# Kernel tuning notes

Measured on AMD Instinct MI355X. Metric: run time of the kernel, lower is better.

## Reference

```python
import jax, jax.numpy as jnp
import numpy as np

NFEATURES = 8192
NPCAS = 256
SIGMA = 16.0
COEFF_NORM = np.sqrt(NPCAS) / SIGMA  # = 1.0
FEAT_NORM = np.sqrt(2.0 / NFEATURES)
TWO_PI = 2.0 * np.pi


def fwht(x):
    """Normalized fast Walsh-Hadamard transform along the last axis (power of 2)."""
    d = x.shape[-1]
    h = 1
    while h < d:
        y = x.reshape(*x.shape[:-1], d // (2 * h), 2, h)
        a, b = y[..., 0, :], y[..., 1, :]
        x = jnp.stack([a + b, a - b], axis=-2).reshape(*x.shape)
        h *= 2
    return x * (d ** -0.5)


def setup_inputs() -> dict:
    key = jax.random.key(0)
    k = jax.random.split(key, 6)
    M, A, R = 32, 64, 512
    S = 4
    nstacks = NFEATURES // NPCAS
    rep = jax.random.normal(k[0], (M, A, R), dtype=jnp.float32)
    charges = jax.random.randint(k[1], (M, A), 0, S, dtype=jnp.int32)
    reductors = jax.random.normal(k[2], (S, R, NPCAS), dtype=jnp.float32)
    Dmat = jax.random.normal(k[3], (S, 1, nstacks, NPCAS), dtype=jnp.float32)
    bias = jax.random.uniform(k[4], (S, NFEATURES), dtype=jnp.float32) * TWO_PI
    alpha = jax.random.normal(k[5], (NFEATURES,), dtype=jnp.float32)
    return {"rep": rep, "charges": charges, "reductors": reductors,
            "Dmat": Dmat, "bias": bias, "alpha": alpha}


def reference(rep, charges, reductors, Dmat, bias, alpha):
    M, A, R = rep.shape
    S, _, P = reductors.shape
    ntransforms, nstacks = Dmat.shape[1], Dmat.shape[2]
    F = nstacks * P
    D = jnp.where(Dmat >= 0, 1.0, -1.0).astype(rep.dtype)  # +-1 SORF diagonals
    Z = jnp.zeros((M, F), dtype=rep.dtype)
    for s in range(S):
        # PCA projection: [M, A, P]
        proj = jnp.einsum('mar,rp->map', rep, reductors[s])
        # replicate across stacks: [M, A, nstacks, P]
        x = jnp.broadcast_to(proj[:, :, None, :], (M, A, nstacks, P))
        for t in range(ntransforms):
            x = fwht(D[s, t] * x)
        coeffs = COEFF_NORM * x.reshape(M, A, F)
        feats = jnp.cos(coeffs + bias[s])
        mask = (charges == s)[..., None]  # species membership per atom
        Z = Z + FEAT_NORM * jnp.sum(jnp.where(mask, feats, 0.0), axis=1)
    return Z @ alpha  # [M] out-of-sample predictions
```

## Files before the change

kernel.cpp:

```cpp
#include <hip/hip_runtime.h>

#define NATOMS 2048
#define R_DIM 512
#define P_DIM 256
#define S_DIM 4
#define NSTACKS 32
#define F_DIM 8192
#define KS 8
#define KSPAN (R_DIM / KS)
#define TR 64
#define TC 128
#define KT 16
#define RT_TILES 11

#define DPPF(x, ctrl) \
  __int_as_float(__builtin_amdgcn_update_dpp( \
      __float_as_int(x), __float_as_int(x), (ctrl), 0xF, 0xF, false))


__global__ __launch_bounds__(256) void sorf_proj_kernel(
    const float* __restrict__ rep, const float* __restrict__ reductors,
    const int* __restrict__ charges, float* __restrict__ projp,
    float* __restrict__ out) {
  int bid = blockIdx.x;
  int ks = bid & 7;
  int cb = (bid >> 3) & 1;
  int r2 = bid >> 4;
  int rt = r2 % RT_TILES;
  int s  = r2 / RT_TILES;

  int t = threadIdx.x;
  int lane = t & 63, wave = t >> 6;
  if (bid == 0 && t < 32) out[t] = 0.f;

  __shared__ int rowsL[TR];
  __shared__ int wtot[4];
  int4 c0v = ((const int4*)charges)[t * 2];
  int4 c1v = ((const int4*)charges)[t * 2 + 1];
  int fl[8];
  fl[0] = (c0v.x == s); fl[1] = (c0v.y == s); fl[2] = (c0v.z == s); fl[3] = (c0v.w == s);
  fl[4] = (c1v.x == s); fl[5] = (c1v.y == s); fl[6] = (c1v.z == s); fl[7] = (c1v.w == s);
  int cnt8 = ((fl[0] + fl[1]) + (fl[2] + fl[3])) + ((fl[4] + fl[5]) + (fl[6] + fl[7]));
  int scan = cnt8;
#pragma unroll
  for (int o = 1; o < 64; o <<= 1) {
    int y = __shfl_up(scan, o);
    if (lane >= o) scan += y;
  }
  if (lane == 63) wtot[wave] = scan;
  __syncthreads();
  int wb = 0;
#pragma unroll
  for (int w = 0; w < 4; ++w) wb += (w < wave) ? wtot[w] : 0;
  int total = (wtot[0] + wtot[1]) + (wtot[2] + wtot[3]);
  int lo = rt * TR;
  int nrows = min(TR, total - lo);
  if (nrows <= 0) return;
  if (t >= nrows && t < TR) rowsL[t] = 0;
  int pos = wb + scan - cnt8;
#pragma unroll
  for (int i = 0; i < 8; ++i) {
    if (fl[i]) {
      int rel = pos - lo;
      if (rel >= 0 && rel < TR) rowsL[rel] = t * 8 + i;
      pos++;
    }
  }
  __syncthreads();

  __shared__ float As[KT][TR + 4];
  __shared__ float Bs[KT][TC];

  int ar = t >> 2;
  int aq = t & 3;
  const float* aSrc = rep + (size_t)rowsL[ar] * R_DIM + ks * KSPAN + aq * 4;
  int kb = t >> 4;
  int cc = (t & 15) * 4;
  const float* bSrc = reductors + ((size_t)s * R_DIM + ks * KSPAN + kb) * P_DIM + cb * TC + cc;

  int ty = t >> 4, tx = t & 15;
  int r0 = ty * 4;
  int c0 = tx * 4;

  float acc[4][8];
#pragma unroll
  for (int i = 0; i < 4; ++i)
#pragma unroll
    for (int j = 0; j < 8; ++j) acc[i][j] = 0.f;

  float4 a  = *(const float4*)aSrc;
  float4 b0 = *(const float4*)bSrc;
  float4 b1 = *(const float4*)(bSrc + 64);

#pragma unroll 1
  for (int k0 = 0; k0 < KSPAN; k0 += KT) {
    __syncthreads();
    As[aq * 4 + 0][ar] = a.x;
    As[aq * 4 + 1][ar] = a.y;
    As[aq * 4 + 2][ar] = a.z;
    As[aq * 4 + 3][ar] = a.w;
    *(float4*)&Bs[kb][cc] = b0;
    *(float4*)&Bs[kb][cc + 64] = b1;
    __syncthreads();
    if (k0 + KT < KSPAN) {
      a  = *(const float4*)(aSrc + k0 + KT);
      b0 = *(const float4*)(bSrc + (size_t)(k0 + KT) * P_DIM);
      b1 = *(const float4*)(bSrc + (size_t)(k0 + KT) * P_DIM + 64);
    }
#pragma unroll
    for (int kk = 0; kk < KT; ++kk) {
      float4 aV = *(const float4*)&As[kk][r0];
      float4 bA = *(const float4*)&Bs[kk][c0];
      float4 bB = *(const float4*)&Bs[kk][c0 + 64];
      float av[4] = {aV.x, aV.y, aV.z, aV.w};
      float bv[8] = {bA.x, bA.y, bA.z, bA.w, bB.x, bB.y, bB.z, bB.w};
#pragma unroll
      for (int i = 0; i < 4; ++i)
#pragma unroll
        for (int j = 0; j < 8; ++j) acc[i][j] = fmaf(av[i], bv[j], acc[i][j]);
    }
  }

#pragma unroll
  for (int i = 0; i < 4; ++i) {
    int r = r0 + i;
    if (r < nrows) {
      float* dst = projp + ((size_t)ks * NATOMS + rowsL[r]) * P_DIM + cb * TC + c0;
      *(float4*)dst = make_float4(acc[i][0], acc[i][1], acc[i][2], acc[i][3]);
      *(float4*)(dst + 64) = make_float4(acc[i][4], acc[i][5], acc[i][6], acc[i][7]);
    }
  }
}

__global__ __launch_bounds__(256) void sorf_feat_kernel(
    const float* __restrict__ projp, const int* __restrict__ charges,
    const float* __restrict__ Dmat, const float* __restrict__ bias,
    const float* __restrict__ alpha, float* __restrict__ out) {
  const int atom = blockIdx.x;
  const int t = threadIdx.x;
  const int lane = t & 63;
  const int wave = t >> 6;
  const int s = charges[atom];

  float4 p = *((const float4*)(projp + (size_t)atom * P_DIM) + lane);
#pragma unroll
  for (int ksi = 1; ksi < KS; ++ksi) {
    float4 q = *((const float4*)(projp + ((size_t)ksi * NATOMS + atom) * P_DIM) + lane);
    p.x += q.x; p.y += q.y; p.z += q.z; p.w += q.w;
  }

  const float sg1  = (lane & 1)  ? -1.f : 1.f;
  const float sg2  = (lane & 2)  ? -1.f : 1.f;
  const float sg4  = (lane & 4)  ? -1.f : 1.f;
  const float sg8  = (lane & 8)  ? -1.f : 1.f;
  const float sg16 = (lane & 16) ? -1.f : 1.f;
  const float sg32 = (lane & 32) ? -1.f : 1.f;
  const bool hi4 = (lane & 4) != 0;

  const float* Db = Dmat + (size_t)s * (NSTACKS * P_DIM);
  const float* bb = bias + (size_t)s * F_DIM;
  float accum = 0.f;

#pragma unroll 2
  for (int j = wave * 8; j < wave * 8 + 8; ++j) {
    float4 d  = *((const float4*)(Db + j * P_DIM) + lane);
    float4 bi = *((const float4*)(bb + j * P_DIM) + lane);
    float4 al = *((const float4*)(alpha + j * P_DIM) + lane);
    float x0 = (d.x >= 0.f) ? p.x : -p.x;
    float x1 = (d.y >= 0.f) ? p.y : -p.y;
    float x2 = (d.z >= 0.f) ? p.z : -p.z;
    float x3 = (d.w >= 0.f) ? p.w : -p.w;
    float t0 = x0 + x1, t1 = x0 - x1, t2 = x2 + x3, t3 = x2 - x3;
    x0 = t0 + t2; x2 = t0 - t2; x1 = t1 + t3; x3 = t1 - t3;
    { float y0 = DPPF(x0, 0xB1), y1 = DPPF(x1, 0xB1), y2 = DPPF(x2, 0xB1), y3 = DPPF(x3, 0xB1);
      x0 = fmaf(sg1, x0, y0); x1 = fmaf(sg1, x1, y1);
      x2 = fmaf(sg1, x2, y2); x3 = fmaf(sg1, x3, y3); }
    { float y0 = DPPF(x0, 0x4E), y1 = DPPF(x1, 0x4E), y2 = DPPF(x2, 0x4E), y3 = DPPF(x3, 0x4E);
      x0 = fmaf(sg2, x0, y0); x1 = fmaf(sg2, x1, y1);
      x2 = fmaf(sg2, x2, y2); x3 = fmaf(sg2, x3, y3); }
    { float a0 = DPPF(x0, 0x104), a1 = DPPF(x1, 0x104), a2 = DPPF(x2, 0x104), a3 = DPPF(x3, 0x104);
      float b0 = DPPF(x0, 0x114), b1 = DPPF(x1, 0x114), b2 = DPPF(x2, 0x114), b3 = DPPF(x3, 0x114);
      float y0 = hi4 ? b0 : a0;
      float y1 = hi4 ? b1 : a1;
      float y2 = hi4 ? b2 : a2;
      float y3 = hi4 ? b3 : a3;
      x0 = fmaf(sg4, x0, y0); x1 = fmaf(sg4, x1, y1);
      x2 = fmaf(sg4, x2, y2); x3 = fmaf(sg4, x3, y3); }
    { float y0 = DPPF(x0, 0x128), y1 = DPPF(x1, 0x128), y2 = DPPF(x2, 0x128), y3 = DPPF(x3, 0x128);
      x0 = fmaf(sg8, x0, y0); x1 = fmaf(sg8, x1, y1);
      x2 = fmaf(sg8, x2, y2); x3 = fmaf(sg8, x3, y3); }
    { float y0 = __shfl_xor(x0, 16), y1 = __shfl_xor(x1, 16),
            y2 = __shfl_xor(x2, 16), y3 = __shfl_xor(x3, 16);
      x0 = fmaf(sg16, x0, y0); x1 = fmaf(sg16, x1, y1);
      x2 = fmaf(sg16, x2, y2); x3 = fmaf(sg16, x3, y3); }
    { float y0 = __shfl_xor(x0, 32), y1 = __shfl_xor(x1, 32),
            y2 = __shfl_xor(x2, 32), y3 = __shfl_xor(x3, 32);
      x0 = fmaf(sg32, x0, y0); x1 = fmaf(sg32, x1, y1);
      x2 = fmaf(sg32, x2, y2); x3 = fmaf(sg32, x3, y3); }
    accum += __cosf(fmaf(x0, 0.0625f, bi.x)) * al.x;
    accum += __cosf(fmaf(x1, 0.0625f, bi.y)) * al.y;
    accum += __cosf(fmaf(x2, 0.0625f, bi.z)) * al.z;
    accum += __cosf(fmaf(x3, 0.0625f, bi.w)) * al.w;
  }

  accum += DPPF(accum, 0xB1);
  accum += DPPF(accum, 0x4E);
  accum += DPPF(accum, 0x124);
  accum += DPPF(accum, 0x128);
  accum += __shfl_xor(accum, 16);
  accum += __shfl_xor(accum, 32);

  __shared__ float wsum[4];
  if (lane == 0) wsum[wave] = accum;
  __syncthreads();
  if (t == 0) {
    atomicAdd(out + (atom >> 6), 0.015625f * ((wsum[0] + wsum[1]) + (wsum[2] + wsum[3])));
  }
}

extern "C" void kernel_launch(void* const* d_in, const int* in_sizes, int n_in,
                              void* d_out, int out_size, void* d_ws, size_t ws_size,
                              hipStream_t stream) {
  const float* rep       = (const float*)d_in[0];
  const int*   charges   = (const int*)d_in[1];
  const float* reductors = (const float*)d_in[2];
  const float* Dmat      = (const float*)d_in[3];
  const float* bias      = (const float*)d_in[4];
  const float* alpha     = (const float*)d_in[5];
  float* out = (float*)d_out;

  float* projp = (float*)((char*)d_ws + 16384);

  sorf_proj_kernel<<<8 * 2 * RT_TILES * S_DIM, 256, 0, stream>>>(
      rep, reductors, charges, projp, out);
  sorf_feat_kernel<<<NATOMS, 256, 0, stream>>>(projp, charges, Dmat, bias, alpha, out);
}
```

Before: 111.0 us.

## Fuse projection and feature kernels into one persistent kernel with grid barrier

Merges the projection GEMM kernel and the SORF feature kernel into a single launch of 704 blocks. A global atomic counter barrier separates the phases, and a memset resets the counter on every call. After the barrier each wave handles one whole atom across all 32 stacks, instead of one block per atom split over four waves. This removes a kernel launch gap and the tail drain between the two kernels. In exchange it adds a memset, a spin barrier that depends on all 704 blocks being co-resident (launch bounds set to 3 blocks per CU), and longer per-wave serial work in the second phase.

Measured after the change: 318.4 us. 2.87x slower.

```diff
diff --git a/kernel.cpp b/kernel.cpp
--- a/kernel.cpp
+++ b/kernel.cpp
@@ -12,209 +12,222 @@
 #define TC 128
 #define KT 16
 #define RT_TILES 11
+#define NTILES (8 * 2 * RT_TILES * S_DIM)
 
 #define DPPF(x, ctrl) \
   __int_as_float(__builtin_amdgcn_update_dpp( \
       __float_as_int(x), __float_as_int(x), (ctrl), 0xF, 0xF, false))
 
 
-__global__ __launch_bounds__(256) void sorf_proj_kernel(
+__global__ __launch_bounds__(256, 3) void sorf_one_kernel(
     const float* __restrict__ rep, const float* __restrict__ reductors,
-    const int* __restrict__ charges, float* __restrict__ projp,
+    const int* __restrict__ charges, const float* __restrict__ Dmat,
+    const float* __restrict__ bias, const float* __restrict__ alpha,
+    float* __restrict__ projp, unsigned* __restrict__ bar,
     float* __restrict__ out) {
-  int bid = blockIdx.x;
-  int ks = bid & 7;
-  int cb = (bid >> 3) & 1;
-  int r2 = bid >> 4;
-  int rt = r2 % RT_TILES;
-  int s  = r2 / RT_TILES;
-
-  int t = threadIdx.x;
-  int lane = t & 63, wave = t >> 6;
-  if (bid == 0 && t < 32) out[t] = 0.f;
-
   __shared__ int rowsL[TR];
   __shared__ int wtot[4];
-  int4 c0v = ((const int4*)charges)[t * 2];
-  int4 c1v = ((const int4*)charges)[t * 2 + 1];
-  int fl[8];
-  fl[0] = (c0v.x == s); fl[1] = (c0v.y == s); fl[2] = (c0v.z == s); fl[3] = (c0v.w == s);
-  fl[4] = (c1v.x == s); fl[5] = (c1v.y == s); fl[6] = (c1v.z == s); fl[7] = (c1v.w == s);
-  int cnt8 = ((fl[0] + fl[1]) + (fl[2] + fl[3])) + ((fl[4] + fl[5]) + (fl[6] + fl[7]));
-  int scan = cnt8;
-#pragma unroll
-  for (int o = 1; o < 64; o <<= 1) {
-    int y = __shfl_up(scan, o);
-    if (lane >= o) scan += y;
-  }
-  if (lane == 63) wtot[wave] = scan;
-  __syncthreads();
-  int wb = 0;
-#pragma unroll
-  for (int w = 0; w < 4; ++w) wb += (w < wave) ? wtot[w] : 0;
-  int total = (wtot[0] + wtot[1]) + (wtot[2] + wtot[3]);
-  int lo = rt * TR;
-  int nrows = min(TR, total - lo);
-  if (nrows <= 0) return;
-  if (t >= nrows && t < TR) rowsL[t] = 0;
-  int pos = wb + scan - cnt8;
-#pragma unroll
-  for (int i = 0; i < 8; ++i) {
-    if (fl[i]) {
-      int rel = pos - lo;
-      if (rel >= 0 && rel < TR) rowsL[rel] = t * 8 + i;
-      pos++;
-    }
-  }
-  __syncthreads();
-
   __shared__ float As[KT][TR + 4];
   __shared__ float Bs[KT][TC];
 
-  int ar = t >> 2;
-  int aq = t & 3;
-  const float* aSrc = rep + (size_t)rowsL[ar] * R_DIM + ks * KSPAN + aq * 4;
-  int kb = t >> 4;
-  int cc = (t & 15) * 4;
-  const float* bSrc = reductors + ((size_t)s * R_DIM + ks * KSPAN + kb) * P_DIM + cb * TC + cc;
-
-  int ty = t >> 4, tx = t & 15;
-  int r0 = ty * 4;
-  int c0 = tx * 4;
-
-  float acc[4][8];
-#pragma unroll
-  for (int i = 0; i < 4; ++i)
-#pragma unroll
-    for (int j = 0; j < 8; ++j) acc[i][j] = 0.f;
-
-  float4 a  = *(const float4*)aSrc;
-  float4 b0 = *(const float4*)bSrc;
-  float4 b1 = *(const float4*)(bSrc + 64);
-
-#pragma unroll 1
-  for (int k0 = 0; k0 < KSPAN; k0 += KT) {
-    __syncthreads();
-    As[aq * 4 + 0][ar] = a.x;
-    As[aq * 4 + 1][ar] = a.y;
-    As[aq * 4 + 2][ar] = a.z;
-    As[aq * 4 + 3][ar] = a.w;
-    *(float4*)&Bs[kb][cc] = b0;
-    *(float4*)&Bs[kb][cc + 64] = b1;
-    __syncthreads();
-    if (k0 + KT < KSPAN) {
-      a  = *(const float4*)(aSrc + k0 + KT);
-      b0 = *(const float4*)(bSrc + (size_t)(k0 + KT) * P_DIM);
-      b1 = *(const float4*)(bSrc + (size_t)(k0 + KT) * P_DIM + 64);
-    }
-#pragma unroll
-    for (int kk = 0; kk < KT; ++kk) {
-      float4 aV = *(const float4*)&As[kk][r0];
-      float4 bA = *(const float4*)&Bs[kk][c0];
-      float4 bB = *(const float4*)&Bs[kk][c0 + 64];
-      float av[4] = {aV.x, aV.y, aV.z, aV.w};
-      float bv[8] = {bA.x, bA.y, bA.z, bA.w, bB.x, bB.y, bB.z, bB.w};
-#pragma unroll
-      for (int i = 0; i < 4; ++i)
-#pragma unroll
-        for (int j = 0; j < 8; ++j) acc[i][j] = fmaf(av[i], bv[j], acc[i][j]);
-    }
-  }
-
-#pragma unroll
-  for (int i = 0; i < 4; ++i) {
-    int r = r0 + i;
-    if (r < nrows) {
-      float* dst = projp + ((size_t)ks * NATOMS + rowsL[r]) * P_DIM + cb * TC + c0;
-      *(float4*)dst = make_float4(acc[i][0], acc[i][1], acc[i][2], acc[i][3]);
-      *(float4*)(dst + 64) = make_float4(acc[i][4], acc[i][5], acc[i][6], acc[i][7]);
-    }
-  }
-}
-
-__global__ __launch_bounds__(256) void sorf_feat_kernel(
-    const float* __restrict__ projp, const int* __restrict__ charges,
-    const float* __restrict__ Dmat, const float* __restrict__ bias,
-    const float* __restrict__ alpha, float* __restrict__ out) {
-  const int atom = blockIdx.x;
   const int t = threadIdx.x;
   const int lane = t & 63;
   const int wave = t >> 6;
-  const int s = charges[atom];
-
-  float4 p = *((const float4*)(projp + (size_t)atom * P_DIM) + lane);
-#pragma unroll
-  for (int ksi = 1; ksi < KS; ++ksi) {
-    float4 q = *((const float4*)(projp + ((size_t)ksi * NATOMS + atom) * P_DIM) + lane);
-    p.x += q.x; p.y += q.y; p.z += q.z; p.w += q.w;
+  const int bid = blockIdx.x;
+
+  if (bid == 0 && t < 32) out[t] = 0.f;
+
+  {
+    int ks = bid & 7;
+    int cb = (bid >> 3) & 1;
+    int r2 = bid >> 4;
+    int rt = r2 % RT_TILES;
+    int s  = r2 / RT_TILES;
+
+    int4 c0v = ((const int4*)charges)[t * 2];
+    int4 c1v = ((const int4*)charges)[t * 2 + 1];
+    int fl[8];
+    fl[0] = (c0v.x == s); fl[1] = (c0v.y == s); fl[2] = (c0v.z == s); fl[3] = (c0v.w == s);
+    fl[4] = (c1v.x == s); fl[5] = (c1v.y == s); fl[6] = (c1v.z == s); fl[7] = (c1v.w == s);
+    int cnt8 = ((fl[0] + fl[1]) + (fl[2] + fl[3])) + ((fl[4] + fl[5]) + (fl[6] + fl[7]));
+    int scan = cnt8;
+#pragma unroll
+    for (int o = 1; o < 64; o <<= 1) {
+      int y = __shfl_up(scan, o);
+      if (lane >= o) scan += y;
+    }
+    if (lane == 63) wtot[wave] = scan;
+    __syncthreads();
+    int wb = 0;
+#pragma unroll
+    for (int w = 0; w < 4; ++w) wb += (w < wave) ? wtot[w] : 0;
+    int total = (wtot[0] + wtot[1]) + (wtot[2] + wtot[3]);
+    int lo = rt * TR;
+    int nrows = min(TR, total - lo);
+    if (nrows > 0) {
+      if (t >= nrows && t < TR) rowsL[t] = 0;
+      int pos = wb + scan - cnt8;
+#pragma unroll
+      for (int i = 0; i < 8; ++i) {
+        if (fl[i]) {
+          int rel = pos - lo;
+          if (rel >= 0 && rel < TR) rowsL[rel] = t * 8 + i;
+          pos++;
+        }
+      }
+      __syncthreads();
+
+      int ar = t >> 2;
+      int aq = t & 3;
+      const float* aSrc = rep + (size_t)rowsL[ar] * R_DIM + ks * KSPAN + aq * 4;
+      int kb = t >> 4;
+      int cc = (t & 15) * 4;
+      const float* bSrc = reductors + ((size_t)s * R_DIM + ks * KSPAN + kb) * P_DIM + cb * TC + cc;
+
+      int ty = t >> 4, tx = t & 15;
+      int r0 = ty * 4;
+      int c0 = tx * 4;
+
+      float acc[4][8];
+#pragma unroll
+      for (int i = 0; i < 4; ++i)
+#pragma unroll
+        for (int j = 0; j < 8; ++j) acc[i][j] = 0.f;
+
+      float4 a  = *(const float4*)aSrc;
+      float4 b0 = *(const float4*)bSrc;
+      float4 b1 = *(const float4*)(bSrc + 64);
+
+#pragma unroll 1
+      for (int k0 = 0; k0 < KSPAN; k0 += KT) {
+        __syncthreads();
+        As[aq * 4 + 0][ar] = a.x;
+        As[aq * 4 + 1][ar] = a.y;
+        As[aq * 4 + 2][ar] = a.z;
+        As[aq * 4 + 3][ar] = a.w;
+        *(float4*)&Bs[kb][cc] = b0;
+        *(float4*)&Bs[kb][cc + 64] = b1;
+        __syncthreads();
+        if (k0 + KT < KSPAN) {
+          a  = *(const float4*)(aSrc + k0 + KT);
+          b0 = *(const float4*)(bSrc + (size_t)(k0 + KT) * P_DIM);
+          b1 = *(const float4*)(bSrc + (size_t)(k0 + KT) * P_DIM + 64);
+        }
+#pragma unroll
+        for (int kk = 0; kk < KT; ++kk) {
+          float4 aV = *(const float4*)&As[kk][r0];
+          float4 bA = *(const float4*)&Bs[kk][c0];
+          float4 bB = *(const float4*)&Bs[kk][c0 + 64];
+          float av[4] = {aV.x, aV.y, aV.z, aV.w};
+          float bv[8] = {bA.x, bA.y, bA.z, bA.w, bB.x, bB.y, bB.z, bB.w};
+#pragma unroll
+          for (int i = 0; i < 4; ++i)
+#pragma unroll
+            for (int j = 0; j < 8; ++j) acc[i][j] = fmaf(av[i], bv[j], acc[i][j]);
+        }
+      }
+
+#pragma unroll
+      for (int i = 0; i < 4; ++i) {
+        int r = r0 + i;
+        if (r < nrows) {
+          float* dst = projp + ((size_t)ks * NATOMS + rowsL[r]) * P_DIM + cb * TC + c0;
+          *(float4*)dst = make_float4(acc[i][0], acc[i][1], acc[i][2], acc[i][3]);
+          *(float4*)(dst + 64) = make_float4(acc[i][4], acc[i][5], acc[i][6], acc[i][7]);
+        }
+      }
+    }
   }
 
-  const float sg1  = (lane & 1)  ? -1.f : 1.f;
-  const float sg2  = (lane & 2)  ? -1.f : 1.f;
-  const float sg4  = (lane & 4)  ? -1.f : 1.f;
-  const float sg8  = (lane & 8)  ? -1.f : 1.f;
-  const float sg16 = (lane & 16) ? -1.f : 1.f;
-  const float sg32 = (lane & 32) ? -1.f : 1.f;
-  const bool hi4 = (lane & 4) != 0;
-
-  const float* Db = Dmat + (size_t)s * (NSTACKS * P_DIM);
-  const float* bb = bias + (size_t)s * F_DIM;
-  float accum = 0.f;
-
-#pragma unroll 2
-  for (int j = wave * 8; j < wave * 8 + 8; ++j) {
-    float4 d  = *((const float4*)(Db + j * P_DIM) + lane);
-    float4 bi = *((const float4*)(bb + j * P_DIM) + lane);
-    float4 al = *((const float4*)(alpha + j * P_DIM) + lane);
-    float x0 = (d.x >= 0.f) ? p.x : -p.x;
-    float x1 = (d.y >= 0.f) ? p.y : -p.y;
-    float x2 = (d.z >= 0.f) ? p.z : -p.z;
-    float x3 = (d.w >= 0.f) ? p.w : -p.w;
-    float t0 = x0 + x1, t1 = x0 - x1, t2 = x2 + x3, t3 = x2 - x3;
-    x0 = t0 + t2; x2 = t0 - t2; x1 = t1 + t3; x3 = t1 - t3;
-    { float y0 = DPPF(x0, 0xB1), y1 = DPPF(x1, 0xB1), y2 = DPPF(x2, 0xB1), y3 = DPPF(x3, 0xB1);
-      x0 = fmaf(sg1, x0, y0); x1 = fmaf(sg1, x1, y1);
-      x2 = fmaf(sg1, x2, y2); x3 = fmaf(sg1, x3, y3); }
-    { float y0 = DPPF(x0, 0x4E), y1 = DPPF(x1, 0x4E), y2 = DPPF(x2, 0x4E), y3 = DPPF(x3, 0x4E);
-      x0 = fmaf(sg2, x0, y0); x1 = fmaf(sg2, x1, y1);
-      x2 = fmaf(sg2, x2, y2); x3 = fmaf(sg2, x3, y3); }
-    { float a0 = DPPF(x0, 0x104), a1 = DPPF(x1, 0x104), a2 = DPPF(x2, 0x104), a3 = DPPF(x3, 0x104);
-      float b0 = DPPF(x0, 0x114), b1 = DPPF(x1, 0x114), b2 = DPPF(x2, 0x114), b3 = DPPF(x3, 0x114);
-      float y0 = hi4 ? b0 : a0;
-      float y1 = hi4 ? b1 : a1;
-      float y2 = hi4 ? b2 : a2;
-      float y3 = hi4 ? b3 : a3;
-      x0 = fmaf(sg4, x0, y0); x1 = fmaf(sg4, x1, y1);
-      x2 = fmaf(sg4, x2, y2); x3 = fmaf(sg4, x3, y3); }
-    { float y0 = DPPF(x0, 0x128), y1 = DPPF(x1, 0x128), y2 = DPPF(x2, 0x128), y3 = DPPF(x3, 0x128);
-      x0 = fmaf(sg8, x0, y0); x1 = fmaf(sg8, x1, y1);
-      x2 = fmaf(sg8, x2, y2); x3 = fmaf(sg8, x3, y3); }
-    { float y0 = __shfl_xor(x0, 16), y1 = __shfl_xor(x1, 16),
-            y2 = __shfl_xor(x2, 16), y3 = __shfl_xor(x3, 16);
-      x0 = fmaf(sg16, x0, y0); x1 = fmaf(sg16, x1, y1);
-      x2 = fmaf(sg16, x2, y2); x3 = fmaf(sg16, x3, y3); }
-    { float y0 = __shfl_xor(x0, 32), y1 = __shfl_xor(x1, 32),
-            y2 = __shfl_xor(x2, 32), y3 = __shfl_xor(x3, 32);
-      x0 = fmaf(sg32, x0, y0); x1 = fmaf(sg32, x1, y1);
-      x2 = fmaf(sg32, x2, y2); x3 = fmaf(sg32, x3, y3); }
-    accum += __cosf(fmaf(x0, 0.0625f, bi.x)) * al.x;
-    accum += __cosf(fmaf(x1, 0.0625f, bi.y)) * al.y;
-    accum += __cosf(fmaf(x2, 0.0625f, bi.z)) * al.z;
-    accum += __cosf(fmaf(x3, 0.0625f, bi.w)) * al.w;
-  }
-
-  accum += DPPF(accum, 0xB1);
-  accum += DPPF(accum, 0x4E);
-  accum += DPPF(accum, 0x124);
-  accum += DPPF(accum, 0x128);
-  accum += __shfl_xor(accum, 16);
-  accum += __shfl_xor(accum, 32);
-
-  __shared__ float wsum[4];
-  if (lane == 0) wsum[wave] = accum;
+  __threadfence();
   __syncthreads();
   if (t == 0) {
-    atomicAdd(out + (atom >> 6), 0.015625f * ((wsum[0] + wsum[1]) + (wsum[2] + wsum[3])));
+    __hip_atomic_fetch_add(bar, 1u, __ATOMIC_RELEASE, __HIP_MEMORY_SCOPE_AGENT);
+    while (__hip_atomic_load(bar, __ATOMIC_ACQUIRE, __HIP_MEMORY_SCOPE_AGENT) <
+           (unsigned)gridDim.x) {
+      __builtin_amdgcn_s_sleep(2);
+    }
+  }
+  __syncthreads();
+  __threadfence();
+
+  {
+    int atom = bid * 4 + wave;
+    if (atom < NATOMS) {
+      const int s = charges[atom];
+
+      float4 p = *((const float4*)(projp + (size_t)atom * P_DIM) + lane);
+#pragma unroll
+      for (int ksi = 1; ksi < KS; ++ksi) {
+        float4 q = *((const float4*)(projp + ((size_t)ksi * NATOMS + atom) * P_DIM) + lane);
+        p.x += q.x; p.y += q.y; p.z += q.z; p.w += q.w;
+      }
+
+      const float sg1  = (lane & 1)  ? -1.f : 1.f;
+      const float sg2  = (lane & 2)  ? -1.f : 1.f;
+      const float sg4  = (lane & 4)  ? -1.f : 1.f;
+      const float sg8  = (lane & 8)  ? -1.f : 1.f;
+      const float sg16 = (lane & 16) ? -1.f : 1.f;
+      const float sg32 = (lane & 32) ? -1.f : 1.f;
+      const bool hi4 = (lane & 4) != 0;
+
+      const float* Db = Dmat + (size_t)s * (NSTACKS * P_DIM);
+      const float* bb = bias + (size_t)s * F_DIM;
+      float accum = 0.f;
+
+#pragma unroll 2
+      for (int j = 0; j < NSTACKS; ++j) {
+        float4 d  = *((const float4*)(Db + j * P_DIM) + lane);
+        float4 bi = *((const float4*)(bb + j * P_DIM) + lane);
+        float4 al = *((const float4*)(alpha + j * P_DIM) + lane);
+        float x0 = (d.x >= 0.f) ? p.x : -p.x;
+        float x1 = (d.y >= 0.f) ? p.y : -p.y;
+        float x2 = (d.z >= 0.f) ? p.z : -p.z;
+        float x3 = (d.w >= 0.f) ? p.w : -p.w;
+        float t0 = x0 + x1, t1 = x0 - x1, t2 = x2 + x3, t3 = x2 - x3;
+        x0 = t0 + t2; x2 = t0 - t2; x1 = t1 + t3; x3 = t1 - t3;
+        { float y0 = DPPF(x0, 0xB1), y1 = DPPF(x1, 0xB1), y2 = DPPF(x2, 0xB1), y3 = DPPF(x3, 0xB1);
+          x0 = fmaf(sg1, x0, y0); x1 = fmaf(sg1, x1, y1);
+          x2 = fmaf(sg1, x2, y2); x3 = fmaf(sg1, x3, y3); }
+        { float y0 = DPPF(x0, 0x4E), y1 = DPPF(x1, 0x4E), y2 = DPPF(x2, 0x4E), y3 = DPPF(x3, 0x4E);
+          x0 = fmaf(sg2, x0, y0); x1 = fmaf(sg2, x1, y1);
+          x2 = fmaf(sg2, x2, y2); x3 = fmaf(sg2, x3, y3); }
+        { float a0 = DPPF(x0, 0x104), a1 = DPPF(x1, 0x104), a2 = DPPF(x2, 0x104), a3 = DPPF(x3, 0x104);
+          float b0 = DPPF(x0, 0x114), b1 = DPPF(x1, 0x114), b2 = DPPF(x2, 0x114), b3 = DPPF(x3, 0x114);
+          float y0 = hi4 ? b0 : a0;
+          float y1 = hi4 ? b1 : a1;
+          float y2 = hi4 ? b2 : a2;
+          float y3 = hi4 ? b3 : a3;
+          x0 = fmaf(sg4, x0, y0); x1 = fmaf(sg4, x1, y1);
+          x2 = fmaf(sg4, x2, y2); x3 = fmaf(sg4, x3, y3); }
+        { float y0 = DPPF(x0, 0x128), y1 = DPPF(x1, 0x128), y2 = DPPF(x2, 0x128), y3 = DPPF(x3, 0x128);
+          x0 = fmaf(sg8, x0, y0); x1 = fmaf(sg8, x1, y1);
+          x2 = fmaf(sg8, x2, y2); x3 = fmaf(sg8, x3, y3); }
+        { float y0 = __shfl_xor(x0, 16), y1 = __shfl_xor(x1, 16),
+                y2 = __shfl_xor(x2, 16), y3 = __shfl_xor(x3, 16);
+          x0 = fmaf(sg16, x0, y0); x1 = fmaf(sg16, x1, y1);
+          x2 = fmaf(sg16, x2, y2); x3 = fmaf(sg16, x3, y3); }
+        { float y0 = __shfl_xor(x0, 32), y1 = __shfl_xor(x1, 32),
+                y2 = __shfl_xor(x2, 32), y3 = __shfl_xor(x3, 32);
+          x0 = fmaf(sg32, x0, y0); x1 = fmaf(sg32, x1, y1);
+          x2 = fmaf(sg32, x2, y2); x3 = fmaf(sg32, x3, y3); }
+        accum += __cosf(fmaf(x0, 0.0625f, bi.x)) * al.x;
+        accum += __cosf(fmaf(x1, 0.0625f, bi.y)) * al.y;
+        accum += __cosf(fmaf(x2, 0.0625f, bi.z)) * al.z;
+        accum += __cosf(fmaf(x3, 0.0625f, bi.w)) * al.w;
+      }
+
+      accum += DPPF(accum, 0xB1);
+      accum += DPPF(accum, 0x4E);
+      accum += DPPF(accum, 0x124);
+      accum += DPPF(accum, 0x128);
+      accum += __shfl_xor(accum, 16);
+      accum += __shfl_xor(accum, 32);
+
+      if (lane == 0) {
+        atomicAdd(out + (atom >> 6), 0.015625f * accum);
+      }
+    }
   }
 }
 
@@ -229,9 +242,10 @@
   const float* alpha     = (const float*)d_in[5];
   float* out = (float*)d_out;
 
-  float* projp = (float*)((char*)d_ws + 16384);
-
-  sorf_proj_kernel<<<8 * 2 * RT_TILES * S_DIM, 256, 0, stream>>>(
-      rep, reductors, charges, projp, out);
-  sorf_feat_kernel<<<NATOMS, 256, 0, stream>>>(projp, charges, Dmat, bias, alpha, out);
+  unsigned* bar  = (unsigned*)((char*)d_ws + 8192);
+  float*   projp = (float*)((char*)d_ws + 16384);
+
+  hipMemsetAsync(bar, 0, 64, stream);
+  sorf_one_kernel<<<NTILES, 256, 0, stream>>>(rep, reductors, charges, Dmat,
+                                              bias, alpha, projp, bar, out);
 }
```
